# Optimization experiments

Measured on AMD Instinct MI355X. Metric: run time of the kernel, lower is better.

The kernel has to match this reference:

```python
import jax, jax.numpy as jnp
import numpy as np

N, E, R = 30000, 300000, 3
IN, HID, OUT, HEADS = 256, 32, 64, 4
NEG_SLOPE = 0.2  # DGL GATConv default


def setup_inputs() -> dict:
    key = jax.random.key(0)
    ks = jax.random.split(key, 10)
    x = jax.random.normal(ks[0], (N, IN), jnp.float32)
    src = jax.random.randint(ks[1], (R, E), 0, N)
    dst = jax.random.randint(ks[2], (R, E), 0, N)
    s1 = (2.0 / IN) ** 0.5
    W1 = jax.random.normal(ks[3], (R, IN, HEADS * HID), jnp.float32) * s1
    attn_l1 = jax.random.normal(ks[4], (R, HEADS, HID), jnp.float32) * 0.1
    attn_r1 = jax.random.normal(ks[5], (R, HEADS, HID), jnp.float32) * 0.1
    b1 = jnp.zeros((R, HEADS * HID), jnp.float32)
    s2 = (2.0 / (HEADS * HID)) ** 0.5
    W2 = jax.random.normal(ks[6], (R, HEADS * HID, HEADS * OUT), jnp.float32) * s2
    attn_l2 = jax.random.normal(ks[7], (R, HEADS, OUT), jnp.float32) * 0.1
    attn_r2 = jax.random.normal(ks[8], (R, HEADS, OUT), jnp.float32) * 0.1
    b2 = jnp.zeros((R, HEADS * OUT), jnp.float32)
    return dict(x=x, src=src, dst=dst, W1=W1, attn_l1=attn_l1, attn_r1=attn_r1,
                b1=b1, W2=W2, attn_l2=attn_l2, attn_r2=attn_r2, b2=b2)


def _gat(x, s, d, W, al, ar, b):
    """Single-relation GATConv (DGL semantics): gather, edge softmax, scatter."""
    n = x.shape[0]
    H, D = al.shape
    z = (x @ W).reshape(n, H, D)                 # [n,H,D]
    el = (z * al[None]).sum(-1)                  # [n,H]
    er = (z * ar[None]).sum(-1)                  # [n,H]
    e = jax.nn.leaky_relu(el[s] + er[d], NEG_SLOPE)   # [E,H]
    m = jax.ops.segment_max(e, d, num_segments=n)     # stable edge softmax per dst
    w = jnp.exp(e - m[d])
    denom = jax.ops.segment_sum(w, d, num_segments=n)
    alpha = w / denom[d]                         # [E,H]
    out = jax.ops.segment_sum(alpha[:, :, None] * z[s], d, num_segments=n)  # [n,H,D]
    return out + b.reshape(1, H, D)


def reference(x, src, dst, W1, attn_l1, attn_r1, b1, W2, attn_l2, attn_r2, b2):
    gat_r = jax.vmap(_gat, in_axes=(None, 0, 0, 0, 0, 0, 0))
    # conv1: per-relation GAT summed across relations (HeteroGraphConv aggregate='sum')
    h = gat_r(x, src, dst, W1, attn_l1, attn_r1, b1).sum(0)      # [N,HEADS,HID]
    h = jax.nn.relu(h).reshape(-1, HEADS * HID)                  # [N,HEADS*HID]
    # conv2
    h2 = gat_r(h, src, dst, W2, attn_l2, attn_r2, b2).sum(0)     # [N,HEADS,OUT]
    return h2.mean(axis=1)                                       # [N,OUT]
```

## Files before the change

### kernel.cpp

```cpp
#include <hip/hip_runtime.h>
#include <math.h>

#define NNODES 30000
#define MPAD   30080
#define NEDGES 300000
#define NREL 3
#define IND 256
#define HIDD 32
#define OUTD 64
#define NHEADS 4
#define C1 (NHEADS*HIDD)
#define C2 (NHEADS*OUTD)
#define NEG_SLOPE 0.2f
#define CAP 64

typedef short bf16x8 __attribute__((ext_vector_type(8)));
typedef float f32x4  __attribute__((ext_vector_type(4)));

__device__ __forceinline__ float b2f(unsigned short u) {
    return __uint_as_float(((unsigned)u) << 16);
}
__device__ __forceinline__ unsigned short f2b(float f) {
    unsigned u = __float_as_uint(f);
    u += 0x7fffu + ((u >> 16) & 1u);
    return (unsigned short)(u >> 16);
}

template<int K, int N>
__device__ __forceinline__ void pack_w_dev(const float* __restrict__ W,
                                           unsigned short* __restrict__ P, int t) {
    const int KS = K / 32, NT = N / 16;
    int lane = t & 63;
    int fid = t >> 6;
    if (fid >= NREL * NT * KS) return;
    int ks = fid % KS;
    int nt = (fid / KS) % NT;
    int r  = fid / (KS * NT);
    int n  = nt * 16 + (lane & 15);
    int k0 = ks * 32 + (lane >> 4) * 8;
    const float* Wr = W + (size_t)r * K * N;
    unsigned short o[8];
#pragma unroll
    for (int j = 0; j < 8; j++) o[j] = f2b(Wr[(size_t)(k0 + j) * N + n]);
    unsigned short* dst = P + (size_t)fid * 512 + lane * 8;
    *(ushort4*)&dst[0] = *(ushort4*)&o[0];
    *(ushort4*)&dst[4] = *(ushort4*)&o[4];
}

#define CAST_BLOCKS (NNODES * IND / 4 / 256)
#define PACK1_BLOCKS (NREL * (C1/16) * (IND/32) / 4)
#define PACK2_BLOCKS (NREL * (C2/16) * (C1/32) / 4)
__global__ void prep_kernel(const float* __restrict__ x, unsigned short* __restrict__ Xh,
                            const float* __restrict__ W1, unsigned short* __restrict__ P1,
                            const float* __restrict__ W2, unsigned short* __restrict__ P2) {
    int b = blockIdx.x;
    if (b < CAST_BLOCKS) {
        int i = (b * 256 + threadIdx.x) * 4;
        float4 v = *(const float4*)&x[i];
        ushort4 o = { f2b(v.x), f2b(v.y), f2b(v.z), f2b(v.w) };
        *(ushort4*)&Xh[i] = o;
    } else if (b < CAST_BLOCKS + PACK1_BLOCKS) {
        pack_w_dev<IND, C1>(W1, P1, (b - CAST_BLOCKS) * 256 + threadIdx.x);
    } else {
        pack_w_dev<C1, C2>(W2, P2, (b - CAST_BLOCKS - PACK1_BLOCKS) * 256 + threadIdx.x);
    }
}

template<int K, int N>
__global__ __launch_bounds__(256) void mfma_gemm(
    const unsigned short* __restrict__ Ah, const unsigned short* __restrict__ Bp,
    const float* __restrict__ al, const float* __restrict__ ar,
    unsigned short* __restrict__ Zh, float* __restrict__ el, float* __restrict__ er)
{
    const int KS = K / 32, NT = N / 16, MT = 64, NP = N + 4;
    const int wave = threadIdx.x >> 6, lane = threadIdx.x & 63;
    const int r  = blockIdx.y;
    const int m0 = blockIdx.x * MT;
    const int fcol = lane & 15, quad = lane >> 4;

    __shared__ unsigned short zs[MT * (N + 4)];

    int m = m0 + wave * 16 + fcol;
    if (m >= NNODES) m = NNODES - 1;
    bf16x8 afrag[KS];
    const unsigned short* arow = Ah + (size_t)m * K + quad * 8;
#pragma unroll
    for (int ks = 0; ks < KS; ks++) afrag[ks] = *(const bf16x8*)(arow + ks * 32);

    f32x4 acc[NT];
#pragma unroll
    for (int nt = 0; nt < NT; nt++) { f32x4 z = {0.f,0.f,0.f,0.f}; acc[nt] = z; }

    const unsigned short* Bpr = Bp + (size_t)r * NT * KS * 512;
    for (int ks = 0; ks < KS; ks++) {
        bf16x8 b[NT];
#pragma unroll
        for (int nt = 0; nt < NT; nt++)
            b[nt] = *(const bf16x8*)(Bpr + ((size_t)nt * KS + ks) * 512 + lane * 8);
#pragma unroll
        for (int nt = 0; nt < NT; nt++)
            acc[nt] = __builtin_amdgcn_mfma_f32_16x16x32_bf16(afrag[ks], b[nt], acc[nt], 0, 0, 0);
    }

    {
        int lrow = wave * 16 + quad * 4;
#pragma unroll
        for (int nt = 0; nt < NT; nt++)
#pragma unroll
            for (int q = 0; q < 4; q++)
                zs[(lrow + q) * NP + nt * 16 + fcol] = f2b(acc[nt][q]);
    }
    __syncthreads();

    {
        uint2* zo = (uint2*)(Zh + ((size_t)r * MPAD + m0) * N);
        for (int i = threadIdx.x; i < MT * N / 4; i += 256) {
            int row = i / (N / 4), c4 = i % (N / 4);
            zo[i] = *(const uint2*)&zs[row * NP + c4 * 4];
        }
    }
    {
        const int D = N / NHEADS;
        int row = threadIdx.x >> 2, h = threadIdx.x & 3;
        int n = m0 + row;
        if (n < NNODES) {
            const float* alp = al + ((size_t)r * NHEADS + h) * D;
            const float* arp = ar + ((size_t)r * NHEADS + h) * D;
            const unsigned short* zp = zs + row * NP + h * D;
            float sl = 0.f, sr = 0.f;
#pragma unroll
            for (int d0 = 0; d0 < D; d0 += 4) {
                uint2 u = *(const uint2*)&zp[d0];
                float z0 = b2f((unsigned short)(u.x & 0xffff));
                float z1 = b2f((unsigned short)(u.x >> 16));
                float z2 = b2f((unsigned short)(u.y & 0xffff));
                float z3 = b2f((unsigned short)(u.y >> 16));
                sl = fmaf(z0, alp[d0], sl);     sr = fmaf(z0, arp[d0], sr);
                sl = fmaf(z1, alp[d0 + 1], sl); sr = fmaf(z1, arp[d0 + 1], sr);
                sl = fmaf(z2, alp[d0 + 2], sl); sr = fmaf(z2, arp[d0 + 2], sr);
                sl = fmaf(z3, alp[d0 + 3], sl); sr = fmaf(z3, arp[d0 + 3], sr);
            }
            el[((size_t)r * NNODES + n) * NHEADS + h] = sl;
            er[((size_t)r * NNODES + n) * NHEADS + h] = sr;
        }
    }
}

__global__ void bucket_fill(const int* __restrict__ src, const int* __restrict__ dst,
                            unsigned* __restrict__ cnt, int* __restrict__ buck) {
    int gid = blockIdx.x * blockDim.x + threadIdx.x;
    if (gid >= NREL * NEDGES) return;
    int r = gid / NEDGES;
    int d = dst[gid];
    int base = r * NNODES + d;
    unsigned pos = atomicAdd(&cnt[base], 1u);
    if (pos < CAP) buck[(size_t)base * CAP + pos] = src[gid];
}

__device__ __forceinline__ float wave_max(float t) {
#pragma unroll
    for (int o = 1; o < 64; o <<= 1) t = fmaxf(t, __shfl_xor(t, o, 64));
    return t;
}
__device__ __forceinline__ float wave_sum(float t) {
#pragma unroll
    for (int o = 1; o < 64; o <<= 1) t += __shfl_xor(t, o, 64);
    return t;
}

__global__ __launch_bounds__(256) void gat_gather1(
    const unsigned* __restrict__ cnt, const int* __restrict__ buck,
    const float* __restrict__ el, const float* __restrict__ er,
    const unsigned short* __restrict__ Zh, const float* __restrict__ b1,
    unsigned short* __restrict__ hbh)
{
    __shared__ float atab[4][4 * 65];
    int wave = threadIdx.x >> 6, lane = threadIdx.x & 63;
    int n = blockIdx.x * 4 + wave;
    if (n >= NNODES) return;
    const int h0 = lane >> 4;
    float accx = 0.f, accy = 0.f;
    for (int r = 0; r < NREL; r++) {
        int base = r * NNODES + n;
        int c = (int)cnt[base]; c = c < CAP ? c : CAP;
        if (c == 0) continue;
        int s_lane = (lane < c) ? buck[(size_t)base * CAP + lane] : -1;
        float lg[4];
        if (s_lane >= 0) {
            const float4 e4 = *(const float4*)&el[((size_t)r * NNODES + s_lane) * NHEADS];
            const float4 r4 = *(const float4*)&er[(size_t)base * NHEADS];
            float v;
            v = e4.x + r4.x; lg[0] = v > 0.f ? v : NEG_SLOPE * v;
            v = e4.y + r4.y; lg[1] = v > 0.f ? v : NEG_SLOPE * v;
            v = e4.z + r4.z; lg[2] = v > 0.f ? v : NEG_SLOPE * v;
            v = e4.w + r4.w; lg[3] = v > 0.f ? v : NEG_SLOPE * v;
        } else {
            lg[0] = lg[1] = lg[2] = lg[3] = -INFINITY;
        }
#pragma unroll
        for (int h = 0; h < 4; h++) {
            float m = wave_max(lg[h]);
            float w = (lane < c) ? __expf(lg[h] - m) : 0.f;
            float den = wave_sum(w);
            atab[wave][h * 65 + lane] = w / den;
        }
        const unsigned short* Zr = Zh + (size_t)r * MPAD * C1;
        const float* at = atab[wave] + h0 * 65;
        int j = 0;
        for (; j + 3 < c; j += 4) {
            int s0 = __builtin_amdgcn_readlane(s_lane, j);
            int s1 = __builtin_amdgcn_readlane(s_lane, j + 1);
            int s2 = __builtin_amdgcn_readlane(s_lane, j + 2);
            int s3 = __builtin_amdgcn_readlane(s_lane, j + 3);
            const ushort2 za = *(const ushort2*)&Zr[(size_t)s0 * C1 + 2 * lane];
            const ushort2 zb = *(const ushort2*)&Zr[(size_t)s1 * C1 + 2 * lane];
            const ushort2 zc = *(const ushort2*)&Zr[(size_t)s2 * C1 + 2 * lane];
            const ushort2 zd = *(const ushort2*)&Zr[(size_t)s3 * C1 + 2 * lane];
            float a0 = at[j], a1 = at[j + 1], a2 = at[j + 2], a3 = at[j + 3];
            accx = fmaf(a0, b2f(za.x), accx); accy = fmaf(a0, b2f(za.y), accy);
            accx = fmaf(a1, b2f(zb.x), accx); accy = fmaf(a1, b2f(zb.y), accy);
            accx = fmaf(a2, b2f(zc.x), accx); accy = fmaf(a2, b2f(zc.y), accy);
            accx = fmaf(a3, b2f(zd.x), accx); accy = fmaf(a3, b2f(zd.y), accy);
        }
        for (; j < c; j++) {
            int s = __builtin_amdgcn_readlane(s_lane, j);
            float a0 = at[j];
            const ushort2 z2 = *(const ushort2*)&Zr[(size_t)s * C1 + 2 * lane];
            accx = fmaf(a0, b2f(z2.x), accx);
            accy = fmaf(a0, b2f(z2.y), accy);
        }
    }
    int cch = 2 * lane;
    float bx = b1[cch]     + b1[C1 + cch]     + b1[2 * C1 + cch];
    float by = b1[cch + 1] + b1[C1 + cch + 1] + b1[2 * C1 + cch + 1];
    ushort2 o;
    o.x = f2b(fmaxf(accx + bx, 0.f));
    o.y = f2b(fmaxf(accy + by, 0.f));
    *(ushort2*)&hbh[(size_t)n * C1 + cch] = o;
}

__global__ __launch_bounds__(256) void gat_gather2(
    const unsigned* __restrict__ cnt, const int* __restrict__ buck,
    const float* __restrict__ el, const float* __restrict__ er,
    const unsigned short* __restrict__ Zh, const float* __restrict__ b2,
    float* __restrict__ out)
{
    __shared__ float atab[4][4 * 65];
    int wave = threadIdx.x >> 6, lane = threadIdx.x & 63;
    int n = blockIdx.x * 4 + wave;
    if (n >= NNODES) return;
    const int h0 = lane >> 4;
    float4 acc = {0.f, 0.f, 0.f, 0.f};
    for (int r = 0; r < NREL; r++) {
        int base = r * NNODES + n;
        int c = (int)cnt[base]; c = c < CAP ? c : CAP;
        if (c == 0) continue;
        int s_lane = (lane < c) ? buck[(size_t)base * CAP + lane] : -1;
        float lg[4];
        if (s_lane >= 0) {
            const float4 e4 = *(const float4*)&el[((size_t)r * NNODES + s_lane) * NHEADS];
            const float4 r4 = *(const float4*)&er[(size_t)base * NHEADS];
            float v;
            v = e4.x + r4.x; lg[0] = v > 0.f ? v : NEG_SLOPE * v;
            v = e4.y + r4.y; lg[1] = v > 0.f ? v : NEG_SLOPE * v;
            v = e4.z + r4.z; lg[2] = v > 0.f ? v : NEG_SLOPE * v;
            v = e4.w + r4.w; lg[3] = v > 0.f ? v : NEG_SLOPE * v;
        } else {
            lg[0] = lg[1] = lg[2] = lg[3] = -INFINITY;
        }
#pragma unroll
        for (int h = 0; h < 4; h++) {
            float m = wave_max(lg[h]);
            float w = (lane < c) ? __expf(lg[h] - m) : 0.f;
            float den = wave_sum(w);
            atab[wave][h * 65 + lane] = w / den;
        }
        const unsigned short* Zr = Zh + (size_t)r * MPAD * C2;
        const float* at = atab[wave] + h0 * 65;
        int j = 0;
        for (; j + 3 < c; j += 4) {
            int s0 = __builtin_amdgcn_readlane(s_lane, j);
            int s1 = __builtin_amdgcn_readlane(s_lane, j + 1);
            int s2 = __builtin_amdgcn_readlane(s_lane, j + 2);
            int s3 = __builtin_amdgcn_readlane(s_lane, j + 3);
            const ushort4 za = *(const ushort4*)&Zr[(size_t)s0 * C2 + 4 * lane];
            const ushort4 zb = *(const ushort4*)&Zr[(size_t)s1 * C2 + 4 * lane];
            const ushort4 zc = *(const ushort4*)&Zr[(size_t)s2 * C2 + 4 * lane];
            const ushort4 zd = *(const ushort4*)&Zr[(size_t)s3 * C2 + 4 * lane];
            float a0 = at[j], a1 = at[j + 1], a2 = at[j + 2], a3 = at[j + 3];
            acc.x = fmaf(a0, b2f(za.x), acc.x); acc.y = fmaf(a0, b2f(za.y), acc.y);
            acc.z = fmaf(a0, b2f(za.z), acc.z); acc.w = fmaf(a0, b2f(za.w), acc.w);
            acc.x = fmaf(a1, b2f(zb.x), acc.x); acc.y = fmaf(a1, b2f(zb.y), acc.y);
            acc.z = fmaf(a1, b2f(zb.z), acc.z); acc.w = fmaf(a1, b2f(zb.w), acc.w);
            acc.x = fmaf(a2, b2f(zc.x), acc.x); acc.y = fmaf(a2, b2f(zc.y), acc.y);
            acc.z = fmaf(a2, b2f(zc.z), acc.z); acc.w = fmaf(a2, b2f(zc.w), acc.w);
            acc.x = fmaf(a3, b2f(zd.x), acc.x); acc.y = fmaf(a3, b2f(zd.y), acc.y);
            acc.z = fmaf(a3, b2f(zd.z), acc.z); acc.w = fmaf(a3, b2f(zd.w), acc.w);
        }
        for (; j < c; j++) {
            int s = __builtin_amdgcn_readlane(s_lane, j);
            float a0 = at[j];
            const ushort4 z4 = *(const ushort4*)&Zr[(size_t)s * C2 + 4 * lane];
            acc.x = fmaf(a0, b2f(z4.x), acc.x);
            acc.y = fmaf(a0, b2f(z4.y), acc.y);
            acc.z = fmaf(a0, b2f(z4.z), acc.z);
            acc.w = fmaf(a0, b2f(z4.w), acc.w);
        }
    }
    int cch = 4 * lane;
#pragma unroll
    for (int q = 0; q < 4; q++) {
        float b = b2[cch + q] + b2[C2 + cch + q] + b2[2 * C2 + cch + q];
        (&acc.x)[q] += b;
    }
    acc.x += __shfl_xor(acc.x, 16, 64); acc.y += __shfl_xor(acc.y, 16, 64);
    acc.z += __shfl_xor(acc.z, 16, 64); acc.w += __shfl_xor(acc.w, 16, 64);
    acc.x += __shfl_xor(acc.x, 32, 64); acc.y += __shfl_xor(acc.y, 32, 64);
    acc.z += __shfl_xor(acc.z, 32, 64); acc.w += __shfl_xor(acc.w, 32, 64);
    if (lane < 16) {
        float4 o;
        o.x = 0.25f * acc.x; o.y = 0.25f * acc.y;
        o.z = 0.25f * acc.z; o.w = 0.25f * acc.w;
        *(float4*)&out[(size_t)n * OUTD + 4 * lane] = o;
    }
}

extern "C" void kernel_launch(void* const* d_in, const int* in_sizes, int n_in,
                              void* d_out, int out_size, void* d_ws, size_t ws_size,
                              hipStream_t stream) {
    (void)in_sizes; (void)n_in; (void)out_size; (void)ws_size;
    const float* x   = (const float*)d_in[0];
    const int*   src = (const int*)d_in[1];
    const int*   dst = (const int*)d_in[2];
    const float* W1  = (const float*)d_in[3];
    const float* al1 = (const float*)d_in[4];
    const float* ar1 = (const float*)d_in[5];
    const float* b1  = (const float*)d_in[6];
    const float* W2  = (const float*)d_in[7];
    const float* al2 = (const float*)d_in[8];
    const float* ar2 = (const float*)d_in[9];
    const float* b2  = (const float*)d_in[10];
    float* out = (float*)d_out;

    float* ws = (float*)d_ws;
    size_t off = 0;
    unsigned short* Zh  = (unsigned short*)(ws + off); off += (size_t)NREL * MPAD * C2 / 2;
    unsigned short* Xh  = (unsigned short*)(ws + off); off += (size_t)NNODES * IND / 2;
    unsigned short* hbh = (unsigned short*)(ws + off); off += (size_t)NNODES * C1 / 2;
    unsigned short* P1  = (unsigned short*)(ws + off); off += (size_t)NREL * (C1/16) * (IND/32) * 512 / 2;
    unsigned short* P2  = (unsigned short*)(ws + off); off += (size_t)NREL * (C2/16) * (C1/32) * 512 / 2;
    float* el  = ws + off; off += (size_t)NREL * NNODES * NHEADS;
    float* er  = ws + off; off += (size_t)NREL * NNODES * NHEADS;
    unsigned* cnt = (unsigned*)(ws + off); off += (size_t)NREL * NNODES;
    int* buck  = (int*)(ws + off); off += (size_t)NREL * NNODES * CAP;

    const int TB = 256;

    hipMemsetAsync(cnt, 0, (size_t)NREL * NNODES * sizeof(unsigned), stream);
    bucket_fill<<<(NREL * NEDGES + TB - 1) / TB, TB, 0, stream>>>(src, dst, cnt, buck);
    prep_kernel<<<CAST_BLOCKS + PACK1_BLOCKS + PACK2_BLOCKS, TB, 0, stream>>>(
        x, Xh, W1, P1, W2, P2);

    {
        dim3 grid(MPAD / 64, NREL);
        mfma_gemm<IND, C1><<<grid, 256, 0, stream>>>(Xh, P1, al1, ar1, Zh, el, er);
    }
    gat_gather1<<<(NNODES + 3) / 4, 256, 0, stream>>>(cnt, buck, el, er, Zh, b1, hbh);

    {
        dim3 grid(MPAD / 64, NREL);
        mfma_gemm<C1, C2><<<grid, 256, 0, stream>>>(hbh, P2, al2, ar2, Zh, el, er);
    }
    gat_gather2<<<(NNODES + 3) / 4, 256, 0, stream>>>(cnt, buck, el, er, Zh, b2, out);
}
```

Baseline: 371.5 us.

## Reassociate layer-2 GAT: aggregate hidden features first, then apply head-collapsed weight

Removes the layer-2 GEMM that materialized Z2 for every node. Attention logits el/er now come from a precomputed W2·attn table applied to the hidden features. The gather kernel aggregates the 128-wide hidden rows per head, then multiplies by a head-mean-collapsed W2 packed for MFMA, with the bias and the head mean folded in. This cuts gather bandwidth from 256-wide bf16 rows to 128-wide rows and drops a full GEMM plus its Z write, at the cost of a per-head aggregation with four times the FMA work and an extra small logits kernel.

```diff
diff --git a/kernel.cpp b/kernel.cpp
--- a/kernel.cpp
+++ b/kernel.cpp
@@ -24,6 +24,9 @@
     unsigned u = __float_as_uint(f);
     u += 0x7fffu + ((u >> 16) & 1u);
     return (unsigned short)(u >> 16);
+}
+__device__ __forceinline__ float rlf(float v, int l) {
+    return __uint_as_float(__builtin_amdgcn_readlane(__float_as_uint(v), l));
 }
 
 template<int K, int N>
@@ -47,12 +50,41 @@
     *(ushort4*)&dst[4] = *(ushort4*)&o[4];
 }
 
+__device__ __forceinline__ void pack_v_dev(const float* __restrict__ W2,
+                                           unsigned short* __restrict__ P, int t) {
+    const int KS = 16, NT = 4;
+    int lane = t & 63;
+    int fid = t >> 6;
+    if (fid >= NREL * NT * KS) return;
+    int ks = fid % KS;
+    int nt = (fid / KS) % NT;
+    int r  = fid / (KS * NT);
+    int n  = nt * 16 + (lane & 15);
+    int k0 = ks * 32 + (lane >> 4) * 8;
+    const float* Wr = W2 + (size_t)r * C1 * C2;
+    unsigned short o[8];
+#pragma unroll
+    for (int j = 0; j < 8; j++) {
+        int k = k0 + j;
+        int c = k & 127, h = k >> 7;
+        o[j] = f2b(Wr[(size_t)c * C2 + h * OUTD + n]);
+    }
+    unsigned short* dst = P + (size_t)fid * 512 + lane * 8;
+    *(ushort4*)&dst[0] = *(ushort4*)&o[0];
+    *(ushort4*)&dst[4] = *(ushort4*)&o[4];
+}
+
 #define CAST_BLOCKS (NNODES * IND / 4 / 256)
 #define PACK1_BLOCKS (NREL * (C1/16) * (IND/32) / 4)
-#define PACK2_BLOCKS (NREL * (C2/16) * (C1/32) / 4)
+#define PACKV_BLOCKS (NREL * 4 * 16 / 4)
+#define VLR_BLOCKS 6
+#define PREP_BLOCKS (CAST_BLOCKS + PACK1_BLOCKS + PACKV_BLOCKS + VLR_BLOCKS + 1)
 __global__ void prep_kernel(const float* __restrict__ x, unsigned short* __restrict__ Xh,
                             const float* __restrict__ W1, unsigned short* __restrict__ P1,
-                            const float* __restrict__ W2, unsigned short* __restrict__ P2) {
+                            const float* __restrict__ W2, unsigned short* __restrict__ PV,
+                            const float* __restrict__ al2, const float* __restrict__ ar2,
+                            const float* __restrict__ bb2,
+                            float* __restrict__ tabs, float* __restrict__ biasout) {
     int b = blockIdx.x;
     if (b < CAST_BLOCKS) {
         int i = (b * 256 + threadIdx.x) * 4;
@@ -61,8 +93,33 @@
         *(ushort4*)&Xh[i] = o;
     } else if (b < CAST_BLOCKS + PACK1_BLOCKS) {
         pack_w_dev<IND, C1>(W1, P1, (b - CAST_BLOCKS) * 256 + threadIdx.x);
+    } else if (b < CAST_BLOCKS + PACK1_BLOCKS + PACKV_BLOCKS) {
+        pack_v_dev(W2, PV, (b - CAST_BLOCKS - PACK1_BLOCKS) * 256 + threadIdx.x);
+    } else if (b < CAST_BLOCKS + PACK1_BLOCKS + PACKV_BLOCKS + VLR_BLOCKS) {
+        int t = (b - CAST_BLOCKS - PACK1_BLOCKS - PACKV_BLOCKS) * 256 + threadIdx.x;
+        if (t < NREL * NHEADS * C1) {
+            int c = t & 127, rh = t >> 7;
+            const float* Wr = W2 + (size_t)(rh >> 2) * C1 * C2 + (size_t)c * C2 + (rh & 3) * OUTD;
+            const float* alp = al2 + (size_t)rh * OUTD;
+            const float* arp = ar2 + (size_t)rh * OUTD;
+            float sl = 0.f, sr = 0.f;
+#pragma unroll 4
+            for (int d = 0; d < OUTD; d++) {
+                sl = fmaf(Wr[d], alp[d], sl);
+                sr = fmaf(Wr[d], arp[d], sr);
+            }
+            tabs[(rh * 2 + 0) * C1 + c] = sl;
+            tabs[(rh * 2 + 1) * C1 + c] = sr;
+        }
     } else {
-        pack_w_dev<C1, C2>(W2, P2, (b - CAST_BLOCKS - PACK1_BLOCKS) * 256 + threadIdx.x);
+        int t = threadIdx.x;
+        if (t < OUTD) {
+            float s = 0.f;
+#pragma unroll
+            for (int rh = 0; rh < NREL * NHEADS; rh++)
+                s += bb2[(size_t)(rh >> 2) * C2 + (rh & 3) * OUTD + t];
+            biasout[t] = 0.25f * s;
+        }
     }
 }
 
@@ -239,89 +296,143 @@
     *(ushort2*)&hbh[(size_t)n * C1 + cch] = o;
 }
 
-__global__ __launch_bounds__(256) void gat_gather2(
+__global__ __launch_bounds__(256) void elr2_kernel(
+    const unsigned short* __restrict__ hbh, const float* __restrict__ tabs,
+    float* __restrict__ el, float* __restrict__ er)
+{
+    int wave = threadIdx.x >> 6, lane = threadIdx.x & 63;
+    int n = blockIdx.x * 4 + wave;
+    unsigned z = *(const unsigned*)&hbh[(size_t)n * C1 + 2 * lane];
+    float z0 = __uint_as_float(z << 16);
+    float z1 = __uint_as_float(z & 0xffff0000u);
+    float p[24];
+#pragma unroll
+    for (int j = 0; j < 24; j++) {
+        float2 t = *(const float2*)&tabs[j * C1 + 2 * lane];
+        p[j] = fmaf(z1, t.y, z0 * t.x);
+    }
+#pragma unroll
+    for (int o = 1; o < 64; o <<= 1) {
+#pragma unroll
+        for (int j = 0; j < 24; j++) p[j] += __shfl_xor(p[j], o, 64);
+    }
+    if (lane == 0) {
+#pragma unroll
+        for (int j = 0; j < 24; j++) {
+            int rh = j >> 1;
+            size_t idx = ((size_t)(rh >> 2) * NNODES + n) * NHEADS + (rh & 3);
+            if (j & 1) er[idx] = p[j]; else el[idx] = p[j];
+        }
+    }
+}
+
+__global__ __launch_bounds__(256) void gat_gather2f(
     const unsigned* __restrict__ cnt, const int* __restrict__ buck,
     const float* __restrict__ el, const float* __restrict__ er,
-    const unsigned short* __restrict__ Zh, const float* __restrict__ b2,
-    float* __restrict__ out)
+    const unsigned short* __restrict__ hbh, const unsigned short* __restrict__ PV,
+    const float* __restrict__ biasout, float* __restrict__ out)
 {
-    __shared__ float atab[4][4 * 65];
-    int wave = threadIdx.x >> 6, lane = threadIdx.x & 63;
-    int n = blockIdx.x * 4 + wave;
-    if (n >= NNODES) return;
-    const int h0 = lane >> 4;
-    float4 acc = {0.f, 0.f, 0.f, 0.f};
+    __shared__ unsigned short aggs[16 * 512];
+    const int wave = threadIdx.x >> 6, lane = threadIdx.x & 63;
+    const int fcol = lane & 15, quad = lane >> 4;
+    const int n0 = blockIdx.x * 16;
+
+    f32x4 acc = {0.f, 0.f, 0.f, 0.f};
+
     for (int r = 0; r < NREL; r++) {
-        int base = r * NNODES + n;
-        int c = (int)cnt[base]; c = c < CAP ? c : CAP;
-        if (c == 0) continue;
-        int s_lane = (lane < c) ? buck[(size_t)base * CAP + lane] : -1;
-        float lg[4];
-        if (s_lane >= 0) {
-            const float4 e4 = *(const float4*)&el[((size_t)r * NNODES + s_lane) * NHEADS];
-            const float4 r4 = *(const float4*)&er[(size_t)base * NHEADS];
-            float v;
-            v = e4.x + r4.x; lg[0] = v > 0.f ? v : NEG_SLOPE * v;
-            v = e4.y + r4.y; lg[1] = v > 0.f ? v : NEG_SLOPE * v;
-            v = e4.z + r4.z; lg[2] = v > 0.f ? v : NEG_SLOPE * v;
-            v = e4.w + r4.w; lg[3] = v > 0.f ? v : NEG_SLOPE * v;
-        } else {
-            lg[0] = lg[1] = lg[2] = lg[3] = -INFINITY;
-        }
-#pragma unroll
-        for (int h = 0; h < 4; h++) {
-            float m = wave_max(lg[h]);
-            float w = (lane < c) ? __expf(lg[h] - m) : 0.f;
-            float den = wave_sum(w);
-            atab[wave][h * 65 + lane] = w / den;
-        }
-        const unsigned short* Zr = Zh + (size_t)r * MPAD * C2;
-        const float* at = atab[wave] + h0 * 65;
-        int j = 0;
-        for (; j + 3 < c; j += 4) {
-            int s0 = __builtin_amdgcn_readlane(s_lane, j);
-            int s1 = __builtin_amdgcn_readlane(s_lane, j + 1);
-            int s2 = __builtin_amdgcn_readlane(s_lane, j + 2);
-            int s3 = __builtin_amdgcn_readlane(s_lane, j + 3);
-            const ushort4 za = *(const ushort4*)&Zr[(size_t)s0 * C2 + 4 * lane];
-            const ushort4 zb = *(const ushort4*)&Zr[(size_t)s1 * C2 + 4 * lane];
-            const ushort4 zc = *(const ushort4*)&Zr[(size_t)s2 * C2 + 4 * lane];
-            const ushort4 zd = *(const ushort4*)&Zr[(size_t)s3 * C2 + 4 * lane];
-            float a0 = at[j], a1 = at[j + 1], a2 = at[j + 2], a3 = at[j + 3];
-            acc.x = fmaf(a0, b2f(za.x), acc.x); acc.y = fmaf(a0, b2f(za.y), acc.y);
-            acc.z = fmaf(a0, b2f(za.z), acc.z); acc.w = fmaf(a0, b2f(za.w), acc.w);
-            acc.x = fmaf(a1, b2f(zb.x), acc.x); acc.y = fmaf(a1, b2f(zb.y), acc.y);
-            acc.z = fmaf(a1, b2f(zb.z), acc.z); acc.w = fmaf(a1, b2f(zb.w), acc.w);
-            acc.x = fmaf(a2, b2f(zc.x), acc.x); acc.y = fmaf(a2, b2f(zc.y), acc.y);
-            acc.z = fmaf(a2, b2f(zc.z), acc.z); acc.w = fmaf(a2, b2f(zc.w), acc.w);
-            acc.x = fmaf(a3, b2f(zd.x), acc.x); acc.y = fmaf(a3, b2f(zd.y), acc.y);
-            acc.z = fmaf(a3, b2f(zd.z), acc.z); acc.w = fmaf(a3, b2f(zd.w), acc.w);
-        }
-        for (; j < c; j++) {
-            int s = __builtin_amdgcn_readlane(s_lane, j);
-            float a0 = at[j];
-            const ushort4 z4 = *(const ushort4*)&Zr[(size_t)s * C2 + 4 * lane];
-            acc.x = fmaf(a0, b2f(z4.x), acc.x);
-            acc.y = fmaf(a0, b2f(z4.y), acc.y);
-            acc.z = fmaf(a0, b2f(z4.z), acc.z);
-            acc.w = fmaf(a0, b2f(z4.w), acc.w);
-        }
-    }
-    int cch = 4 * lane;
+        float ag[4][8];
+#pragma unroll
+        for (int i = 0; i < 4; i++)
+#pragma unroll
+            for (int k = 0; k < 8; k++) ag[i][k] = 0.f;
+
+#pragma unroll
+        for (int i = 0; i < 4; i++) {
+            int n = n0 + wave * 4 + i;
+            int base = r * NNODES + n;
+            int c = (int)cnt[base]; c = c < CAP ? c : CAP;
+            if (c == 0) continue;
+            int s_lane = (lane < c) ? buck[(size_t)base * CAP + lane] : -1;
+            float lg[4];
+            if (s_lane >= 0) {
+                const float4 e4 = *(const float4*)&el[((size_t)r * NNODES + s_lane) * NHEADS];
+                const float4 r4 = *(const float4*)&er[(size_t)base * NHEADS];
+                float v;
+                v = e4.x + r4.x; lg[0] = v > 0.f ? v : NEG_SLOPE * v;
+                v = e4.y + r4.y; lg[1] = v > 0.f ? v : NEG_SLOPE * v;
+                v = e4.z + r4.z; lg[2] = v > 0.f ? v : NEG_SLOPE * v;
+                v = e4.w + r4.w; lg[3] = v > 0.f ? v : NEG_SLOPE * v;
+            } else {
+                lg[0] = lg[1] = lg[2] = lg[3] = -INFINITY;
+            }
+            float aw[4];
+#pragma unroll
+            for (int h = 0; h < 4; h++) {
+                float m = wave_max(lg[h]);
+                float w = (lane < c) ? __expf(lg[h] - m) : 0.f;
+                float den = wave_sum(w);
+                aw[h] = w / den;
+            }
+#define EDGE1(zz, jj)                                                           \
+            {   float a0 = rlf(aw[0], jj), a1 = rlf(aw[1], jj);                 \
+                float a2 = rlf(aw[2], jj), a3 = rlf(aw[3], jj);                 \
+                float z0 = __uint_as_float((zz) << 16);                         \
+                float z1 = __uint_as_float((zz) & 0xffff0000u);                 \
+                ag[i][0] = fmaf(a0, z0, ag[i][0]); ag[i][1] = fmaf(a0, z1, ag[i][1]); \
+                ag[i][2] = fmaf(a1, z0, ag[i][2]); ag[i][3] = fmaf(a1, z1, ag[i][3]); \
+                ag[i][4] = fmaf(a2, z0, ag[i][4]); ag[i][5] = fmaf(a2, z1, ag[i][5]); \
+                ag[i][6] = fmaf(a3, z0, ag[i][6]); ag[i][7] = fmaf(a3, z1, ag[i][7]); }
+            int j = 0;
+            for (; j + 3 < c; j += 4) {
+                int s0 = __builtin_amdgcn_readlane(s_lane, j);
+                int s1 = __builtin_amdgcn_readlane(s_lane, j + 1);
+                int s2 = __builtin_amdgcn_readlane(s_lane, j + 2);
+                int s3 = __builtin_amdgcn_readlane(s_lane, j + 3);
+                unsigned za = *(const unsigned*)&hbh[(size_t)s0 * C1 + 2 * lane];
+                unsigned zb = *(const unsigned*)&hbh[(size_t)s1 * C1 + 2 * lane];
+                unsigned zc = *(const unsigned*)&hbh[(size_t)s2 * C1 + 2 * lane];
+                unsigned zd = *(const unsigned*)&hbh[(size_t)s3 * C1 + 2 * lane];
+                EDGE1(za, j); EDGE1(zb, j + 1); EDGE1(zc, j + 2); EDGE1(zd, j + 3);
+            }
+            for (; j < c; j++) {
+                int s = __builtin_amdgcn_readlane(s_lane, j);
+                unsigned zz = *(const unsigned*)&hbh[(size_t)s * C1 + 2 * lane];
+                EDGE1(zz, j);
+            }
+#undef EDGE1
+        }
+
+        __syncthreads();
+#pragma unroll
+        for (int i = 0; i < 4; i++) {
+            int row = wave * 4 + i;
+            unsigned sw = (unsigned)((row & 7) << 4);
+            char* basep = (char*)aggs + row * 1024;
+#pragma unroll
+            for (int h = 0; h < 4; h++) {
+                unsigned pk = ((unsigned)f2b(ag[i][2 * h + 1]) << 16) | f2b(ag[i][2 * h]);
+                *(unsigned*)(basep + (((unsigned)(h * 256 + lane * 4)) ^ sw)) = pk;
+            }
+        }
+        __syncthreads();
+
+        const unsigned short* PVr = PV + ((size_t)(r * 4 + wave) * 16) * 512;
+#pragma unroll
+        for (int ks = 0; ks < 16; ks++) {
+            bf16x8 b = *(const bf16x8*)(PVr + (size_t)ks * 512 + lane * 8);
+            const char* ap = (const char*)aggs + fcol * 1024 +
+                             (((unsigned)(ks * 64 + quad * 16)) ^ ((unsigned)((fcol & 7) << 4)));
+            bf16x8 a = *(const bf16x8*)ap;
+            acc = __builtin_amdgcn_mfma_f32_16x16x32_bf16(a, b, acc, 0, 0, 0);
+        }
+    }
+
+    int col = wave * 16 + fcol;
+    float bias = biasout[col];
 #pragma unroll
     for (int q = 0; q < 4; q++) {
-        float b = b2[cch + q] + b2[C2 + cch + q] + b2[2 * C2 + cch + q];
-        (&acc.x)[q] += b;
-    }
-    acc.x += __shfl_xor(acc.x, 16, 64); acc.y += __shfl_xor(acc.y, 16, 64);
-    acc.z += __shfl_xor(acc.z, 16, 64); acc.w += __shfl_xor(acc.w, 16, 64);
-    acc.x += __shfl_xor(acc.x, 32, 64); acc.y += __shfl_xor(acc.y, 32, 64);
-    acc.z += __shfl_xor(acc.z, 32, 64); acc.w += __shfl_xor(acc.w, 32, 64);
-    if (lane < 16) {
-        float4 o;
-        o.x = 0.25f * acc.x; o.y = 0.25f * acc.y;
-        o.z = 0.25f * acc.z; o.w = 0.25f * acc.w;
-        *(float4*)&out[(size_t)n * OUTD + 4 * lane] = o;
+        int row = n0 + quad * 4 + q;
+        out[(size_t)row * OUTD + col] = fmaf(0.25f, acc[q], bias);
     }
 }
 
@@ -348,18 +459,20 @@
     unsigned short* Xh  = (unsigned short*)(ws + off); off += (size_t)NNODES * IND / 2;
     unsigned short* hbh = (unsigned short*)(ws + off); off += (size_t)NNODES * C1 / 2;
     unsigned short* P1  = (unsigned short*)(ws + off); off += (size_t)NREL * (C1/16) * (IND/32) * 512 / 2;
-    unsigned short* P2  = (unsigned short*)(ws + off); off += (size_t)NREL * (C2/16) * (C1/32) * 512 / 2;
+    unsigned short* PV  = (unsigned short*)(ws + off); off += (size_t)NREL * 4 * 16 * 512 / 2;
     float* el  = ws + off; off += (size_t)NREL * NNODES * NHEADS;
     float* er  = ws + off; off += (size_t)NREL * NNODES * NHEADS;
     unsigned* cnt = (unsigned*)(ws + off); off += (size_t)NREL * NNODES;
     int* buck  = (int*)(ws + off); off += (size_t)NREL * NNODES * CAP;
+    float* tabs    = ws + off; off += 24 * C1;
+    float* biasout = ws + off; off += OUTD;
 
     const int TB = 256;
 
     hipMemsetAsync(cnt, 0, (size_t)NREL * NNODES * sizeof(unsigned), stream);
     bucket_fill<<<(NREL * NEDGES + TB - 1) / TB, TB, 0, stream>>>(src, dst, cnt, buck);
-    prep_kernel<<<CAST_BLOCKS + PACK1_BLOCKS + PACK2_BLOCKS, TB, 0, stream>>>(
-        x, Xh, W1, P1, W2, P2);
+    prep_kernel<<<PREP_BLOCKS, TB, 0, stream>>>(x, Xh, W1, P1, W2, PV, al2, ar2, b2,
+                                                tabs, biasout);
 
     {
         dim3 grid(MPAD / 64, NREL);
@@ -367,9 +480,6 @@
     }
     gat_gather1<<<(NNODES + 3) / 4, 256, 0, stream>>>(cnt, buck, el, er, Zh, b1, hbh);
 
-    {
-        dim3 grid(MPAD / 64, NREL);
-        mfma_gemm<C1, C2><<<grid, 256, 0, stream>>>(hbh, P2, al2, ar2, Zh, el, er);
-    }
-    gat_gather2<<<(NNODES + 3) / 4, 256, 0, stream>>>(cnt, buck, el, er, Zh, b2, out);
-}
+    elr2_kernel<<<NNODES / 4, 256, 0, stream>>>(hbh, tabs, el, er);
+    gat_gather2f<<<NNODES / 16, 256, 0, stream>>>(cnt, buck, el, er, hbh, PV, biasout, out);
+}
```

Result: slower. 407.4 us (+9.7%).
